# Optimization experiments

Hardware: AMD Instinct MI355X
Metric: run time of the kernel (lower is better)

The kernel has to match this reference:

```python
import jax, jax.numpy as jnp
import numpy as np

B, R, C, NC = 8, 1000, 1024, 81
H, W = 1024, 1024
MEANS = jnp.array([0.0, 0.0, 0.0, 0.0], jnp.float32)
STDS = jnp.array([0.1, 0.1, 0.2, 0.2], jnp.float32)
MIN_CONF = 0.05
NMS_THR = 0.5
MAX_INST = 100
NEG = -1e9


def setup_inputs() -> dict:
    key = jax.random.key(0)
    k1, k2, k3, k4, k5 = jax.random.split(key, 5)
    x = jax.random.normal(k1, (B * R, C), jnp.float32)
    w_cls = jax.random.normal(k2, (C, NC), jnp.float32) * 0.01
    b_cls = jnp.zeros((NC,), jnp.float32)
    w_delta = jax.random.normal(k3, (C, 4), jnp.float32) * 0.01
    b_delta = jnp.zeros((4,), jnp.float32)
    # rois: (batch_ind, y1, x1, y2, x2), normalized coords with y1<y2, x1<x2
    yx1 = jax.random.uniform(k4, (B * R, 2), jnp.float32) * 0.7
    hw = jax.random.uniform(k5, (B * R, 2), jnp.float32) * 0.28 + 0.02
    bind = jnp.repeat(jnp.arange(B, dtype=jnp.float32), R)[:, None]
    rois = jnp.concatenate([bind, yx1, yx1 + hw], axis=1)
    return {"x": x, "w_cls": w_cls, "b_cls": b_cls, "w_delta": w_delta, "b_delta": b_delta, "rois": rois}


def delta2bbox(rois, deltas):
    # rois, deltas: [N, 4] in (y1, x1, y2, x2) / (dy, dx, dh, dw)
    d = deltas * STDS + MEANS
    h = rois[:, 2] - rois[:, 0]
    w = rois[:, 3] - rois[:, 1]
    cy = rois[:, 0] + 0.5 * h + d[:, 0] * h
    cx = rois[:, 1] + 0.5 * w + d[:, 1] * w
    h = h * jnp.exp(d[:, 2])
    w = w * jnp.exp(d[:, 3])
    return jnp.stack([cy - 0.5 * h, cx - 0.5 * w, cy + 0.5 * h, cx + 0.5 * w], axis=1)


def pairwise_iou(boxes):
    # boxes: [N, 4]
    area = (boxes[:, 2] - boxes[:, 0]) * (boxes[:, 3] - boxes[:, 1])
    y1 = jnp.maximum(boxes[:, None, 0], boxes[None, :, 0])
    x1 = jnp.maximum(boxes[:, None, 1], boxes[None, :, 1])
    y2 = jnp.minimum(boxes[:, None, 2], boxes[None, :, 2])
    x2 = jnp.minimum(boxes[:, None, 3], boxes[None, :, 3])
    inter = jnp.maximum(y2 - y1, 0.0) * jnp.maximum(x2 - x1, 0.0)
    union = area[:, None] + area[None, :] - inter
    return inter / jnp.maximum(union, 1e-8)


def nms_single(boxes, scores, class_ids, valid):
    # boxes [R,4], scores [R], class_ids [R] int, valid [R] bool -> detections [MAX_INST, 6]
    masked = jnp.where(valid, scores, NEG)
    order = jnp.argsort(-masked)  # descending score
    b = boxes[order]
    s = masked[order]
    c = class_ids[order]
    v = valid[order]
    # class-aware IoU: cross-class pairs never suppress each other
    iou = pairwise_iou(b) * (c[:, None] == c[None, :]).astype(boxes.dtype)
    n = b.shape[0]

    def step(supp, xs):
        i, iou_row, vi = xs
        keep_i = vi & ~supp[i]
        supp = supp | jnp.where(keep_i, iou_row > NMS_THR, False)
        return supp, keep_i

    _, keep = jax.lax.scan(step, jnp.zeros((n,), bool), (jnp.arange(n), iou, v))
    final = jnp.where(keep, s, NEG)
    top_s, top_i = jax.lax.top_k(final, MAX_INST)
    ok = (top_s > NEG / 2)[:, None]
    det = jnp.concatenate([b[top_i], c[top_i].astype(boxes.dtype)[:, None], s[top_i][:, None]], axis=1)
    return jnp.where(ok, det, 0.0)


def reference(x, w_cls, b_cls, w_delta, b_delta, rois):
    logits = x @ w_cls + b_cls                      # [B*R, NC]
    probs = jax.nn.softmax(logits, axis=-1)
    deltas = x @ w_delta + b_delta                  # [B*R, 4]

    probs_b = probs.reshape(B, R, NC)
    class_ids = jnp.argmax(probs_b, axis=-1).astype(jnp.int32)           # [B, R]
    class_scores = jnp.take_along_axis(probs_b, class_ids[..., None], axis=-1)[..., 0]

    scale = jnp.array([H, W, H, W], jnp.float32)
    boxes = rois[:, 1:5] * scale                    # pixel coords, [B*R, 4]
    refined = delta2bbox(boxes, deltas)
    window = jnp.array([0.0, 0.0, float(H), float(W)], jnp.float32)
    refined = jnp.clip(refined, window[jnp.array([0, 1, 0, 1])], window[jnp.array([2, 3, 2, 3])])
    refined = refined.reshape(B, R, 4)

    valid = (class_ids > 0) & (class_scores >= MIN_CONF)
    detections = jax.vmap(nms_single)(refined, class_scores, class_ids, valid)  # [B, MAX_INST, 6]
    return detections
```

## Files before the change

kernel.cpp:

```cpp
#include <hip/hip_runtime.h>
#include <math.h>
#include <stdint.h>

#define RR 1000
#define CC 1024
#define NCLS 81
#define HH 1024.0f
#define MIN_CONF_V 0.05f
#define NMS_THR_V 0.5f
#define NEGV -1e9f

#define KSTRIDE 520

typedef __attribute__((ext_vector_type(8))) short bf16x8;
typedef __attribute__((ext_vector_type(16))) float f32x16;

__device__ __forceinline__ unsigned short f2bf(float f) {
    unsigned int u = __float_as_uint(f);
    return (unsigned short)((u + 0x7FFFu + ((u >> 16) & 1u)) >> 16);
}
__device__ __forceinline__ float bf2f(unsigned short h) {
    return __uint_as_float(((unsigned int)h) << 16);
}

__global__ __launch_bounds__(64) void k0_pack(
    const float* __restrict__ w_cls, const float* __restrict__ w_delta,
    unsigned short* __restrict__ wh, unsigned short* __restrict__ wl)
{
    const int ct = blockIdx.x >> 6;
    const int ks = blockIdx.x & 63;
    const int l = threadIdx.x;
    const int col = ct * 32 + (l & 31);
    const int kbase = ks * 16 + (l >> 5) * 8;
    unsigned short h[8], lo[8];
    #pragma unroll
    for (int j = 0; j < 8; ++j) {
        const int k = kbase + j;
        float v = 0.f;
        if (col < NCLS)          v = w_cls[(size_t)k * NCLS + col];
        else if (col < NCLS + 4) v = w_delta[(size_t)k * 4 + (col - NCLS)];
        h[j] = f2bf(v);
        lo[j] = f2bf(v - bf2f(h[j]));
    }
    const size_t base = ((size_t)(ct * 64 + ks) * 64 + l) * 8;
    uint4 uh, ul;
    uh.x = (unsigned)h[0] | ((unsigned)h[1] << 16);
    uh.y = (unsigned)h[2] | ((unsigned)h[3] << 16);
    uh.z = (unsigned)h[4] | ((unsigned)h[5] << 16);
    uh.w = (unsigned)h[6] | ((unsigned)h[7] << 16);
    ul.x = (unsigned)lo[0] | ((unsigned)lo[1] << 16);
    ul.y = (unsigned)lo[2] | ((unsigned)lo[3] << 16);
    ul.z = (unsigned)lo[4] | ((unsigned)lo[5] << 16);
    ul.w = (unsigned)lo[6] | ((unsigned)lo[7] << 16);
    *(uint4*)&wh[base] = uh;
    *(uint4*)&wl[base] = ul;
}

__global__ __launch_bounds__(384) void k1_head(
    const float* __restrict__ x,
    const unsigned short* __restrict__ wh, const unsigned short* __restrict__ wl,
    const float* __restrict__ b_cls, const float* __restrict__ b_delta,
    const float* __restrict__ rois,
    float* __restrict__ bx_ws, float* __restrict__ sc_ws, float* __restrict__ cid_ws)
{
    __shared__ __align__(16) unsigned short XH[64 * KSTRIDE];
    __shared__ __align__(16) unsigned short XL[64 * KSTRIDE];

    const int t = threadIdx.x;
    const int lane = t & 63;
    const int wid = t >> 6;
    const int ct = wid >> 1;
    const int half = wid & 1;
    const int row0 = blockIdx.x * 32;

    #pragma unroll
    for (int batch = 0; batch < 2; ++batch) {
        float4 v[11];
        #pragma unroll
        for (int i = 0; i < 11; ++i) {
            const int s = t + (batch * 11 + i) * 384;
            if (s < 8192)
                v[i] = *(const float4*)(x + (size_t)(row0 + (s >> 8)) * CC + (s & 255) * 4);
        }
        #pragma unroll
        for (int i = 0; i < 11; ++i) {
            const int s = t + (batch * 11 + i) * 384;
            if (s < 8192) {
                const int row = s >> 8;
                const int f4 = s & 255;
                const int ks = f4 >> 2;
                const int q = f4 & 3;
                const int lane_ = ((q >> 1) << 5) + row;
                const int j0 = (q & 1) * 4;
                const size_t us = (size_t)ks * KSTRIDE + lane_ * 8 + j0;
                const unsigned short h0 = f2bf(v[i].x), h1 = f2bf(v[i].y),
                                     h2 = f2bf(v[i].z), h3 = f2bf(v[i].w);
                *(ushort4*)&XH[us] = make_ushort4(h0, h1, h2, h3);
                *(ushort4*)&XL[us] = make_ushort4(
                    f2bf(v[i].x - bf2f(h0)), f2bf(v[i].y - bf2f(h1)),
                    f2bf(v[i].z - bf2f(h2)), f2bf(v[i].w - bf2f(h3)));
            }
        }
    }
    __syncthreads();

    const int ks0 = half * 32;
    const unsigned short* whp = wh + (((size_t)ct * 64 + ks0) * 64 + lane) * 8;
    const unsigned short* wlp = wl + (((size_t)ct * 64 + ks0) * 64 + lane) * 8;
    const unsigned short* ap  = &XH[(size_t)ks0 * KSTRIDE + lane * 8];
    const unsigned short* alp = &XL[(size_t)ks0 * KSTRIDE + lane * 8];

    f32x16 acc = {0.f,0.f,0.f,0.f,0.f,0.f,0.f,0.f,0.f,0.f,0.f,0.f,0.f,0.f,0.f,0.f};

    bf16x8 BH[4], BL[4];
    #pragma unroll
    for (int i = 0; i < 4; ++i) {
        BH[i] = *(const bf16x8*)(whp + (size_t)i * 512);
        BL[i] = *(const bf16x8*)(wlp + (size_t)i * 512);
    }

    #pragma unroll
    for (int ks = 0; ks < 32; ++ks) {
        const bf16x8 bh = BH[ks & 3];
        const bf16x8 bl = BL[ks & 3];
        if (ks + 4 < 32) {
            BH[ks & 3] = *(const bf16x8*)(whp + (size_t)(ks + 4) * 512);
            BL[ks & 3] = *(const bf16x8*)(wlp + (size_t)(ks + 4) * 512);
        }
        const bf16x8 ah = *(const bf16x8*)(ap  + (size_t)ks * KSTRIDE);
        const bf16x8 al = *(const bf16x8*)(alp + (size_t)ks * KSTRIDE);
        acc = __builtin_amdgcn_mfma_f32_32x32x16_bf16(ah, bh, acc, 0, 0, 0);
        acc = __builtin_amdgcn_mfma_f32_32x32x16_bf16(ah, bl, acc, 0, 0, 0);
        acc = __builtin_amdgcn_mfma_f32_32x32x16_bf16(al, bh, acc, 0, 0, 0);
    }
    __syncthreads();

    float* outH = (float*)XH;
    float* outT = outH + 3200;
    float* dst = half ? outT : outH;
    const int col = lane & 31;
    #pragma unroll
    for (int reg = 0; reg < 16; ++reg) {
        const int row = (reg & 3) + 8 * (reg >> 2) + 4 * (lane >> 5);
        dst[row * 100 + ct * 32 + col] = acc[reg];
    }
    __syncthreads();

    if (t < 256) {
        const int row = t >> 3;
        const int e = t & 7;
        float vmax = -INFINITY;
        int imax = 1 << 20;
        float vv[12];
        #pragma unroll
        for (int s = 0; s < 12; ++s) {
            const int cidx = e + 8 * s;
            if (cidx < NCLS) {
                const float val = outH[row * 100 + cidx] + outT[row * 100 + cidx] + b_cls[cidx];
                vv[s] = val;
                if (val > vmax) { vmax = val; imax = cidx; }
            } else vv[s] = -INFINITY;
        }
        #pragma unroll
        for (int mm = 4; mm >= 1; mm >>= 1) {
            const float v2 = __shfl_xor(vmax, mm);
            const int   i2 = __shfl_xor(imax, mm);
            if (v2 > vmax || (v2 == vmax && i2 < imax)) { vmax = v2; imax = i2; }
        }
        float sume = 0.f;
        #pragma unroll
        for (int s = 0; s < 12; ++s) {
            const int cidx = e + 8 * s;
            if (cidx < NCLS) sume += expf(vv[s] - vmax);
        }
        #pragma unroll
        for (int mm = 4; mm >= 1; mm >>= 1) sume += __shfl_xor(sume, mm);

        if (e == 0) {
            const int gr = row0 + row;
            const float score = 1.0f / sume;
            const int cid = imax;
            const float d0 = (outH[row * 100 + 81] + outT[row * 100 + 81] + b_delta[0]) * 0.1f;
            const float d1 = (outH[row * 100 + 82] + outT[row * 100 + 82] + b_delta[1]) * 0.1f;
            const float d2 = (outH[row * 100 + 83] + outT[row * 100 + 83] + b_delta[2]) * 0.2f;
            const float d3 = (outH[row * 100 + 84] + outT[row * 100 + 84] + b_delta[3]) * 0.2f;
            const float y1 = rois[(size_t)gr * 5 + 1] * HH;
            const float x1 = rois[(size_t)gr * 5 + 2] * HH;
            const float y2 = rois[(size_t)gr * 5 + 3] * HH;
            const float x2 = rois[(size_t)gr * 5 + 4] * HH;
            const float h = y2 - y1, w = x2 - x1;
            const float cy = y1 + 0.5f * h + d0 * h;
            const float cx = x1 + 0.5f * w + d1 * w;
            const float h2 = h * expf(d2);
            const float w2 = w * expf(d3);
            const float by1 = fminf(fmaxf(cy - 0.5f * h2, 0.f), HH);
            const float bx1 = fminf(fmaxf(cx - 0.5f * w2, 0.f), HH);
            const float by2 = fminf(fmaxf(cy + 0.5f * h2, 0.f), HH);
            const float bx2 = fminf(fmaxf(cx + 0.5f * w2, 0.f), HH);
            const bool valid = (cid > 0) && (score >= MIN_CONF_V);
            bx_ws[(size_t)gr * 4 + 0] = by1;
            bx_ws[(size_t)gr * 4 + 1] = bx1;
            bx_ws[(size_t)gr * 4 + 2] = by2;
            bx_ws[(size_t)gr * 4 + 3] = bx2;
            sc_ws[gr]  = valid ? score : NEGV;
            cid_ws[gr] = (float)cid;
        }
    }
}

__global__ __launch_bounds__(256) void k2_nms(
    const float* __restrict__ bx_ws, const float* __restrict__ sc_ws,
    const float* __restrict__ cid_ws, float* __restrict__ det)
{
    __shared__ unsigned long long keys[256];
    __shared__ float sy1[256], sx1[256], sy2[256], sx2[256];
    __shared__ float scl[256], ssc[256];
    __shared__ unsigned char supp[256];
    __shared__ int s_cnt, s_num;

    const int b = blockIdx.x;
    const int t = threadIdx.x;
    const int base = b * RR;

    keys[t] = 0ull;
    if (t == 0) { s_cnt = 0; s_num = 0; }
    __syncthreads();

    for (int rr = t; rr < RR; rr += 256) {
        const float s = sc_ws[base + rr];
        if (s > NEGV * 0.5f) {
            const int i = atomicAdd(&s_num, 1);
            if (i < 256) {
                unsigned int u = __float_as_uint(s) | 0x80000000u;
                keys[i] = ((unsigned long long)u << 32) | (unsigned int)(~(unsigned int)rr);
            }
        }
    }
    __syncthreads();
    const int V = (s_num < 256) ? s_num : 256;

    for (int k = 2; k <= 256; k <<= 1) {
        for (int j = k >> 1; j > 0; j >>= 1) {
            const int ixj = t ^ j;
            if (ixj > t) {
                const unsigned long long a = keys[t];
                const unsigned long long c = keys[ixj];
                const bool desc = ((t & k) == 0);
                if (desc ? (a < c) : (a > c)) { keys[t] = c; keys[ixj] = a; }
            }
            __syncthreads();
        }
    }

    if (t < V) {
        const int orig = (int)(~(unsigned int)keys[t]);
        const int g = base + orig;
        sy1[t] = bx_ws[(size_t)g * 4 + 0];
        sx1[t] = bx_ws[(size_t)g * 4 + 1];
        sy2[t] = bx_ws[(size_t)g * 4 + 2];
        sx2[t] = bx_ws[(size_t)g * 4 + 3];
        scl[t] = cid_ws[g];
        ssc[t] = sc_ws[g];
    } else {
        sy1[t] = sx1[t] = sy2[t] = sx2[t] = 0.f;
        scl[t] = -1.f;
        ssc[t] = NEGV;
    }
    supp[t] = 0;
    __syncthreads();

    for (int i = 0; i < V; ++i) {
        __syncthreads();
        if (s_cnt >= 100) break;
        if (!supp[i]) {
            if (t > i && t < V && scl[t] == scl[i]) {
                const float yy1 = fmaxf(sy1[i], sy1[t]);
                const float xx1 = fmaxf(sx1[i], sx1[t]);
                const float yy2 = fminf(sy2[i], sy2[t]);
                const float xx2 = fminf(sx2[i], sx2[t]);
                const float inter = fmaxf(yy2 - yy1, 0.f) * fmaxf(xx2 - xx1, 0.f);
                const float ai = (sy2[i] - sy1[i]) * (sx2[i] - sx1[i]);
                const float at = (sy2[t] - sy1[t]) * (sx2[t] - sx1[t]);
                const float uni = ai + at - inter;
                if (inter / fmaxf(uni, 1e-8f) > NMS_THR_V) supp[t] = 1;
            }
            if (t == 0) {
                const int slot = s_cnt;
                if (slot < 100) {
                    float* o = det + ((size_t)b * 100 + slot) * 6;
                    o[0] = sy1[i]; o[1] = sx1[i]; o[2] = sy2[i]; o[3] = sx2[i];
                    o[4] = scl[i]; o[5] = ssc[i];
                }
                s_cnt = slot + 1;
            }
        }
    }
    __syncthreads();
    int cnt = s_cnt;
    if (cnt > 100) cnt = 100;
    for (int idx = t; idx < 600; idx += 256) {
        if (idx >= cnt * 6) det[(size_t)b * 600 + idx] = 0.f;
    }
}

extern "C" void kernel_launch(void* const* d_in, const int* in_sizes, int n_in,
                              void* d_out, int out_size, void* d_ws, size_t ws_size,
                              hipStream_t stream) {
    const float* x       = (const float*)d_in[0];
    const float* w_cls   = (const float*)d_in[1];
    const float* b_cls   = (const float*)d_in[2];
    const float* w_delta = (const float*)d_in[3];
    const float* b_delta = (const float*)d_in[4];
    const float* rois    = (const float*)d_in[5];
    float* out = (float*)d_out;

    float* bx_ws   = (float*)d_ws;
    float* sc_ws   = bx_ws + 8000 * 4;
    float* cid_ws  = sc_ws + 8000;
    unsigned short* wh = (unsigned short*)(cid_ws + 8000);
    unsigned short* wl = wh + 98304;

    k0_pack<<<192, 64, 0, stream>>>(w_cls, w_delta, wh, wl);
    k1_head<<<250, 384, 0, stream>>>(x, wh, wl, b_cls, b_delta, rois,
                                     bx_ws, sc_ws, cid_ws);
    k2_nms<<<8, 256, 0, stream>>>(bx_ws, sc_ws, cid_ws, out);
}
```

Before: 30.70 us.

## Fuse pack, head GEMM and NMS into one cooperative kernel with grid syncs

Merges the three separate launches (weight packing, MFMA head with softmax and box decode, per-image NMS) into a single cooperative kernel of 250 blocks, separated by grid-wide barriers. NMS runs on the first 8 blocks and reuses the head's shared memory buffer. The goal is to remove two kernel launch gaps and their inter-kernel drain. In exchange it adds two grid.sync costs and leaves 242 blocks idle during NMS, and it requires all 250 blocks to be co-resident.

After: 80.49 us. +162.2%, slower.

```diff
diff --git a/kernel.cpp b/kernel.cpp
--- a/kernel.cpp
+++ b/kernel.cpp
@@ -1,6 +1,9 @@
 #include <hip/hip_runtime.h>
+#include <hip/hip_cooperative_groups.h>
 #include <math.h>
 #include <stdint.h>
+
+namespace cg = cooperative_groups;
 
 #define RR 1000
 #define CC 1024
@@ -23,283 +26,300 @@
     return __uint_as_float(((unsigned int)h) << 16);
 }
 
-__global__ __launch_bounds__(64) void k0_pack(
+__global__ __launch_bounds__(384, 1) void fused_all(
+    const float* __restrict__ x,
     const float* __restrict__ w_cls, const float* __restrict__ w_delta,
-    unsigned short* __restrict__ wh, unsigned short* __restrict__ wl)
-{
-    const int ct = blockIdx.x >> 6;
-    const int ks = blockIdx.x & 63;
-    const int l = threadIdx.x;
-    const int col = ct * 32 + (l & 31);
-    const int kbase = ks * 16 + (l >> 5) * 8;
-    unsigned short h[8], lo[8];
-    #pragma unroll
-    for (int j = 0; j < 8; ++j) {
-        const int k = kbase + j;
-        float v = 0.f;
-        if (col < NCLS)          v = w_cls[(size_t)k * NCLS + col];
-        else if (col < NCLS + 4) v = w_delta[(size_t)k * 4 + (col - NCLS)];
-        h[j] = f2bf(v);
-        lo[j] = f2bf(v - bf2f(h[j]));
-    }
-    const size_t base = ((size_t)(ct * 64 + ks) * 64 + l) * 8;
-    uint4 uh, ul;
-    uh.x = (unsigned)h[0] | ((unsigned)h[1] << 16);
-    uh.y = (unsigned)h[2] | ((unsigned)h[3] << 16);
-    uh.z = (unsigned)h[4] | ((unsigned)h[5] << 16);
-    uh.w = (unsigned)h[6] | ((unsigned)h[7] << 16);
-    ul.x = (unsigned)lo[0] | ((unsigned)lo[1] << 16);
-    ul.y = (unsigned)lo[2] | ((unsigned)lo[3] << 16);
-    ul.z = (unsigned)lo[4] | ((unsigned)lo[5] << 16);
-    ul.w = (unsigned)lo[6] | ((unsigned)lo[7] << 16);
-    *(uint4*)&wh[base] = uh;
-    *(uint4*)&wl[base] = ul;
-}
-
-__global__ __launch_bounds__(384) void k1_head(
-    const float* __restrict__ x,
-    const unsigned short* __restrict__ wh, const unsigned short* __restrict__ wl,
     const float* __restrict__ b_cls, const float* __restrict__ b_delta,
     const float* __restrict__ rois,
-    float* __restrict__ bx_ws, float* __restrict__ sc_ws, float* __restrict__ cid_ws)
+    unsigned short* __restrict__ wh, unsigned short* __restrict__ wl,
+    float* __restrict__ bx_ws, float* __restrict__ sc_ws, float* __restrict__ cid_ws,
+    float* __restrict__ det)
 {
     __shared__ __align__(16) unsigned short XH[64 * KSTRIDE];
     __shared__ __align__(16) unsigned short XL[64 * KSTRIDE];
 
     const int t = threadIdx.x;
-    const int lane = t & 63;
-    const int wid = t >> 6;
-    const int ct = wid >> 1;
-    const int half = wid & 1;
-    const int row0 = blockIdx.x * 32;
-
-    #pragma unroll
-    for (int batch = 0; batch < 2; ++batch) {
-        float4 v[11];
+    const int b = blockIdx.x;
+    cg::grid_group grid = cg::this_grid();
+
+    {
+        const int g = b * 384 + t;
+        if (g < 12288) {
+            const int lane = g & 63;
+            const int blk = g >> 6;
+            const int ct = blk >> 6;
+            const int ks = blk & 63;
+            const int col = ct * 32 + (lane & 31);
+            const int kbase = ks * 16 + (lane >> 5) * 8;
+            unsigned short h[8], lo[8];
+            #pragma unroll
+            for (int j = 0; j < 8; ++j) {
+                const int k = kbase + j;
+                float v = 0.f;
+                if (col < NCLS)          v = w_cls[(size_t)k * NCLS + col];
+                else if (col < NCLS + 4) v = w_delta[(size_t)k * 4 + (col - NCLS)];
+                h[j] = f2bf(v);
+                lo[j] = f2bf(v - bf2f(h[j]));
+            }
+            const size_t base = ((size_t)blk * 64 + lane) * 8;
+            uint4 uh, ul;
+            uh.x = (unsigned)h[0] | ((unsigned)h[1] << 16);
+            uh.y = (unsigned)h[2] | ((unsigned)h[3] << 16);
+            uh.z = (unsigned)h[4] | ((unsigned)h[5] << 16);
+            uh.w = (unsigned)h[6] | ((unsigned)h[7] << 16);
+            ul.x = (unsigned)lo[0] | ((unsigned)lo[1] << 16);
+            ul.y = (unsigned)lo[2] | ((unsigned)lo[3] << 16);
+            ul.z = (unsigned)lo[4] | ((unsigned)lo[5] << 16);
+            ul.w = (unsigned)lo[6] | ((unsigned)lo[7] << 16);
+            *(uint4*)&wh[base] = uh;
+            *(uint4*)&wl[base] = ul;
+        }
+    }
+    grid.sync();
+
+    {
+        const int lane = t & 63;
+        const int wid = t >> 6;
+        const int ct = wid >> 1;
+        const int half = wid & 1;
+        const int row0 = b * 32;
+
         #pragma unroll
-        for (int i = 0; i < 11; ++i) {
-            const int s = t + (batch * 11 + i) * 384;
-            if (s < 8192)
-                v[i] = *(const float4*)(x + (size_t)(row0 + (s >> 8)) * CC + (s & 255) * 4);
-        }
+        for (int batch = 0; batch < 2; ++batch) {
+            float4 v[11];
+            #pragma unroll
+            for (int i = 0; i < 11; ++i) {
+                const int s = t + (batch * 11 + i) * 384;
+                if (s < 8192)
+                    v[i] = *(const float4*)(x + (size_t)(row0 + (s >> 8)) * CC + (s & 255) * 4);
+            }
+            #pragma unroll
+            for (int i = 0; i < 11; ++i) {
+                const int s = t + (batch * 11 + i) * 384;
+                if (s < 8192) {
+                    const int row = s >> 8;
+                    const int f4 = s & 255;
+                    const int ks = f4 >> 2;
+                    const int q = f4 & 3;
+                    const int lane_ = ((q >> 1) << 5) + row;
+                    const int j0 = (q & 1) * 4;
+                    const size_t us = (size_t)ks * KSTRIDE + lane_ * 8 + j0;
+                    const unsigned short h0 = f2bf(v[i].x), h1 = f2bf(v[i].y),
+                                         h2 = f2bf(v[i].z), h3 = f2bf(v[i].w);
+                    *(ushort4*)&XH[us] = make_ushort4(h0, h1, h2, h3);
+                    *(ushort4*)&XL[us] = make_ushort4(
+                        f2bf(v[i].x - bf2f(h0)), f2bf(v[i].y - bf2f(h1)),
+                        f2bf(v[i].z - bf2f(h2)), f2bf(v[i].w - bf2f(h3)));
+                }
+            }
+        }
+        __syncthreads();
+
+        const int ks0 = half * 32;
+        const unsigned short* whp = wh + (((size_t)ct * 64 + ks0) * 64 + lane) * 8;
+        const unsigned short* wlp = wl + (((size_t)ct * 64 + ks0) * 64 + lane) * 8;
+        const unsigned short* ap  = &XH[(size_t)ks0 * KSTRIDE + lane * 8];
+        const unsigned short* alp = &XL[(size_t)ks0 * KSTRIDE + lane * 8];
+
+        f32x16 acc = {0.f,0.f,0.f,0.f,0.f,0.f,0.f,0.f,0.f,0.f,0.f,0.f,0.f,0.f,0.f,0.f};
+
+        bf16x8 BH[4], BL[4];
         #pragma unroll
-        for (int i = 0; i < 11; ++i) {
-            const int s = t + (batch * 11 + i) * 384;
-            if (s < 8192) {
-                const int row = s >> 8;
-                const int f4 = s & 255;
-                const int ks = f4 >> 2;
-                const int q = f4 & 3;
-                const int lane_ = ((q >> 1) << 5) + row;
-                const int j0 = (q & 1) * 4;
-                const size_t us = (size_t)ks * KSTRIDE + lane_ * 8 + j0;
-                const unsigned short h0 = f2bf(v[i].x), h1 = f2bf(v[i].y),
-                                     h2 = f2bf(v[i].z), h3 = f2bf(v[i].w);
-                *(ushort4*)&XH[us] = make_ushort4(h0, h1, h2, h3);
-                *(ushort4*)&XL[us] = make_ushort4(
-                    f2bf(v[i].x - bf2f(h0)), f2bf(v[i].y - bf2f(h1)),
-                    f2bf(v[i].z - bf2f(h2)), f2bf(v[i].w - bf2f(h3)));
+        for (int i = 0; i < 4; ++i) {
+            BH[i] = *(const bf16x8*)(whp + (size_t)i * 512);
+            BL[i] = *(const bf16x8*)(wlp + (size_t)i * 512);
+        }
+
+        #pragma unroll
+        for (int ks = 0; ks < 32; ++ks) {
+            const bf16x8 bh = BH[ks & 3];
+            const bf16x8 bl = BL[ks & 3];
+            if (ks + 4 < 32) {
+                BH[ks & 3] = *(const bf16x8*)(whp + (size_t)(ks + 4) * 512);
+                BL[ks & 3] = *(const bf16x8*)(wlp + (size_t)(ks + 4) * 512);
+            }
+            const bf16x8 ah = *(const bf16x8*)(ap  + (size_t)ks * KSTRIDE);
+            const bf16x8 al = *(const bf16x8*)(alp + (size_t)ks * KSTRIDE);
+            acc = __builtin_amdgcn_mfma_f32_32x32x16_bf16(ah, bh, acc, 0, 0, 0);
+            acc = __builtin_amdgcn_mfma_f32_32x32x16_bf16(ah, bl, acc, 0, 0, 0);
+            acc = __builtin_amdgcn_mfma_f32_32x32x16_bf16(al, bh, acc, 0, 0, 0);
+        }
+        __syncthreads();
+
+        float* outH = (float*)XH;
+        float* outT = outH + 3200;
+        float* dst = half ? outT : outH;
+        const int col = lane & 31;
+        #pragma unroll
+        for (int reg = 0; reg < 16; ++reg) {
+            const int row = (reg & 3) + 8 * (reg >> 2) + 4 * (lane >> 5);
+            dst[row * 100 + ct * 32 + col] = acc[reg];
+        }
+        __syncthreads();
+
+        if (t < 256) {
+            const int row = t >> 3;
+            const int e = t & 7;
+            float vmax = -INFINITY;
+            int imax = 1 << 20;
+            float vv[12];
+            #pragma unroll
+            for (int s = 0; s < 12; ++s) {
+                const int cidx = e + 8 * s;
+                if (cidx < NCLS) {
+                    const float val = outH[row * 100 + cidx] + outT[row * 100 + cidx] + b_cls[cidx];
+                    vv[s] = val;
+                    if (val > vmax) { vmax = val; imax = cidx; }
+                } else vv[s] = -INFINITY;
+            }
+            #pragma unroll
+            for (int mm = 4; mm >= 1; mm >>= 1) {
+                const float v2 = __shfl_xor(vmax, mm);
+                const int   i2 = __shfl_xor(imax, mm);
+                if (v2 > vmax || (v2 == vmax && i2 < imax)) { vmax = v2; imax = i2; }
+            }
+            float sume = 0.f;
+            #pragma unroll
+            for (int s = 0; s < 12; ++s) {
+                const int cidx = e + 8 * s;
+                if (cidx < NCLS) sume += expf(vv[s] - vmax);
+            }
+            #pragma unroll
+            for (int mm = 4; mm >= 1; mm >>= 1) sume += __shfl_xor(sume, mm);
+
+            if (e == 0) {
+                const int gr = row0 + row;
+                const float score = 1.0f / sume;
+                const int cid = imax;
+                const float d0 = (outH[row * 100 + 81] + outT[row * 100 + 81] + b_delta[0]) * 0.1f;
+                const float d1 = (outH[row * 100 + 82] + outT[row * 100 + 82] + b_delta[1]) * 0.1f;
+                const float d2 = (outH[row * 100 + 83] + outT[row * 100 + 83] + b_delta[2]) * 0.2f;
+                const float d3 = (outH[row * 100 + 84] + outT[row * 100 + 84] + b_delta[3]) * 0.2f;
+                const float y1 = rois[(size_t)gr * 5 + 1] * HH;
+                const float x1 = rois[(size_t)gr * 5 + 2] * HH;
+                const float y2 = rois[(size_t)gr * 5 + 3] * HH;
+                const float x2 = rois[(size_t)gr * 5 + 4] * HH;
+                const float h = y2 - y1, w = x2 - x1;
+                const float cy = y1 + 0.5f * h + d0 * h;
+                const float cx = x1 + 0.5f * w + d1 * w;
+                const float h2 = h * expf(d2);
+                const float w2 = w * expf(d3);
+                const float by1 = fminf(fmaxf(cy - 0.5f * h2, 0.f), HH);
+                const float bx1 = fminf(fmaxf(cx - 0.5f * w2, 0.f), HH);
+                const float by2 = fminf(fmaxf(cy + 0.5f * h2, 0.f), HH);
+                const float bx2 = fminf(fmaxf(cx + 0.5f * w2, 0.f), HH);
+                const bool valid = (cid > 0) && (score >= MIN_CONF_V);
+                bx_ws[(size_t)gr * 4 + 0] = by1;
+                bx_ws[(size_t)gr * 4 + 1] = bx1;
+                bx_ws[(size_t)gr * 4 + 2] = by2;
+                bx_ws[(size_t)gr * 4 + 3] = bx2;
+                sc_ws[gr]  = valid ? score : NEGV;
+                cid_ws[gr] = (float)cid;
             }
         }
     }
-    __syncthreads();
-
-    const int ks0 = half * 32;
-    const unsigned short* whp = wh + (((size_t)ct * 64 + ks0) * 64 + lane) * 8;
-    const unsigned short* wlp = wl + (((size_t)ct * 64 + ks0) * 64 + lane) * 8;
-    const unsigned short* ap  = &XH[(size_t)ks0 * KSTRIDE + lane * 8];
-    const unsigned short* alp = &XL[(size_t)ks0 * KSTRIDE + lane * 8];
-
-    f32x16 acc = {0.f,0.f,0.f,0.f,0.f,0.f,0.f,0.f,0.f,0.f,0.f,0.f,0.f,0.f,0.f,0.f};
-
-    bf16x8 BH[4], BL[4];
-    #pragma unroll
-    for (int i = 0; i < 4; ++i) {
-        BH[i] = *(const bf16x8*)(whp + (size_t)i * 512);
-        BL[i] = *(const bf16x8*)(wlp + (size_t)i * 512);
-    }
-
-    #pragma unroll
-    for (int ks = 0; ks < 32; ++ks) {
-        const bf16x8 bh = BH[ks & 3];
-        const bf16x8 bl = BL[ks & 3];
-        if (ks + 4 < 32) {
-            BH[ks & 3] = *(const bf16x8*)(whp + (size_t)(ks + 4) * 512);
-            BL[ks & 3] = *(const bf16x8*)(wlp + (size_t)(ks + 4) * 512);
-        }
-        const bf16x8 ah = *(const bf16x8*)(ap  + (size_t)ks * KSTRIDE);
-        const bf16x8 al = *(const bf16x8*)(alp + (size_t)ks * KSTRIDE);
-        acc = __builtin_amdgcn_mfma_f32_32x32x16_bf16(ah, bh, acc, 0, 0, 0);
-        acc = __builtin_amdgcn_mfma_f32_32x32x16_bf16(ah, bl, acc, 0, 0, 0);
-        acc = __builtin_amdgcn_mfma_f32_32x32x16_bf16(al, bh, acc, 0, 0, 0);
-    }
-    __syncthreads();
-
-    float* outH = (float*)XH;
-    float* outT = outH + 3200;
-    float* dst = half ? outT : outH;
-    const int col = lane & 31;
-    #pragma unroll
-    for (int reg = 0; reg < 16; ++reg) {
-        const int row = (reg & 3) + 8 * (reg >> 2) + 4 * (lane >> 5);
-        dst[row * 100 + ct * 32 + col] = acc[reg];
-    }
-    __syncthreads();
-
-    if (t < 256) {
-        const int row = t >> 3;
-        const int e = t & 7;
-        float vmax = -INFINITY;
-        int imax = 1 << 20;
-        float vv[12];
-        #pragma unroll
-        for (int s = 0; s < 12; ++s) {
-            const int cidx = e + 8 * s;
-            if (cidx < NCLS) {
-                const float val = outH[row * 100 + cidx] + outT[row * 100 + cidx] + b_cls[cidx];
-                vv[s] = val;
-                if (val > vmax) { vmax = val; imax = cidx; }
-            } else vv[s] = -INFINITY;
-        }
-        #pragma unroll
-        for (int mm = 4; mm >= 1; mm >>= 1) {
-            const float v2 = __shfl_xor(vmax, mm);
-            const int   i2 = __shfl_xor(imax, mm);
-            if (v2 > vmax || (v2 == vmax && i2 < imax)) { vmax = v2; imax = i2; }
-        }
-        float sume = 0.f;
-        #pragma unroll
-        for (int s = 0; s < 12; ++s) {
-            const int cidx = e + 8 * s;
-            if (cidx < NCLS) sume += expf(vv[s] - vmax);
-        }
-        #pragma unroll
-        for (int mm = 4; mm >= 1; mm >>= 1) sume += __shfl_xor(sume, mm);
-
-        if (e == 0) {
-            const int gr = row0 + row;
-            const float score = 1.0f / sume;
-            const int cid = imax;
-            const float d0 = (outH[row * 100 + 81] + outT[row * 100 + 81] + b_delta[0]) * 0.1f;
-            const float d1 = (outH[row * 100 + 82] + outT[row * 100 + 82] + b_delta[1]) * 0.1f;
-            const float d2 = (outH[row * 100 + 83] + outT[row * 100 + 83] + b_delta[2]) * 0.2f;
-            const float d3 = (outH[row * 100 + 84] + outT[row * 100 + 84] + b_delta[3]) * 0.2f;
-            const float y1 = rois[(size_t)gr * 5 + 1] * HH;
-            const float x1 = rois[(size_t)gr * 5 + 2] * HH;
-            const float y2 = rois[(size_t)gr * 5 + 3] * HH;
-            const float x2 = rois[(size_t)gr * 5 + 4] * HH;
-            const float h = y2 - y1, w = x2 - x1;
-            const float cy = y1 + 0.5f * h + d0 * h;
-            const float cx = x1 + 0.5f * w + d1 * w;
-            const float h2 = h * expf(d2);
-            const float w2 = w * expf(d3);
-            const float by1 = fminf(fmaxf(cy - 0.5f * h2, 0.f), HH);
-            const float bx1 = fminf(fmaxf(cx - 0.5f * w2, 0.f), HH);
-            const float by2 = fminf(fmaxf(cy + 0.5f * h2, 0.f), HH);
-            const float bx2 = fminf(fmaxf(cx + 0.5f * w2, 0.f), HH);
-            const bool valid = (cid > 0) && (score >= MIN_CONF_V);
-            bx_ws[(size_t)gr * 4 + 0] = by1;
-            bx_ws[(size_t)gr * 4 + 1] = bx1;
-            bx_ws[(size_t)gr * 4 + 2] = by2;
-            bx_ws[(size_t)gr * 4 + 3] = bx2;
-            sc_ws[gr]  = valid ? score : NEGV;
-            cid_ws[gr] = (float)cid;
-        }
-    }
-}
-
-__global__ __launch_bounds__(256) void k2_nms(
-    const float* __restrict__ bx_ws, const float* __restrict__ sc_ws,
-    const float* __restrict__ cid_ws, float* __restrict__ det)
-{
-    __shared__ unsigned long long keys[256];
-    __shared__ float sy1[256], sx1[256], sy2[256], sx2[256];
-    __shared__ float scl[256], ssc[256];
-    __shared__ unsigned char supp[256];
-    __shared__ int s_cnt, s_num;
-
-    const int b = blockIdx.x;
-    const int t = threadIdx.x;
-    const int base = b * RR;
-
-    keys[t] = 0ull;
-    if (t == 0) { s_cnt = 0; s_num = 0; }
-    __syncthreads();
-
-    for (int rr = t; rr < RR; rr += 256) {
-        const float s = sc_ws[base + rr];
-        if (s > NEGV * 0.5f) {
-            const int i = atomicAdd(&s_num, 1);
-            if (i < 256) {
-                unsigned int u = __float_as_uint(s) | 0x80000000u;
-                keys[i] = ((unsigned long long)u << 32) | (unsigned int)(~(unsigned int)rr);
-            }
-        }
-    }
-    __syncthreads();
-    const int V = (s_num < 256) ? s_num : 256;
-
-    for (int k = 2; k <= 256; k <<= 1) {
-        for (int j = k >> 1; j > 0; j >>= 1) {
-            const int ixj = t ^ j;
-            if (ixj > t) {
-                const unsigned long long a = keys[t];
-                const unsigned long long c = keys[ixj];
-                const bool desc = ((t & k) == 0);
-                if (desc ? (a < c) : (a > c)) { keys[t] = c; keys[ixj] = a; }
-            }
+    grid.sync();
+
+    if (b < 8) {
+        float* fb = (float*)XH;
+        unsigned long long* keys = (unsigned long long*)fb;
+        float* sy1 = fb + 512;
+        float* sx1 = fb + 768;
+        float* sy2 = fb + 1024;
+        float* sx2 = fb + 1280;
+        float* scl = fb + 1536;
+        float* ssc = fb + 1792;
+        unsigned char* supp = (unsigned char*)(fb + 2048);
+        int* s_cnt = (int*)(fb + 2112);
+        int* s_num = (int*)(fb + 2113);
+
+        const int base = b * RR;
+
+        if (t < 256) keys[t] = 0ull;
+        if (t == 0) { *s_cnt = 0; *s_num = 0; }
+        __syncthreads();
+
+        for (int rr = t; rr < RR; rr += 384) {
+            const float s = sc_ws[base + rr];
+            if (s > NEGV * 0.5f) {
+                const int i = atomicAdd(s_num, 1);
+                if (i < 256) {
+                    unsigned int u = __float_as_uint(s) | 0x80000000u;
+                    keys[i] = ((unsigned long long)u << 32) | (unsigned int)(~(unsigned int)rr);
+                }
+            }
+        }
+        __syncthreads();
+        const int V = (*s_num < 256) ? *s_num : 256;
+
+        if (V > 1) {
+            for (int k = 2; k <= 256; k <<= 1) {
+                for (int j = k >> 1; j > 0; j >>= 1) {
+                    if (t < 256) {
+                        const int ixj = t ^ j;
+                        if (ixj > t) {
+                            const unsigned long long a = keys[t];
+                            const unsigned long long c = keys[ixj];
+                            const bool desc = ((t & k) == 0);
+                            if (desc ? (a < c) : (a > c)) { keys[t] = c; keys[ixj] = a; }
+                        }
+                    }
+                    __syncthreads();
+                }
+            }
+        }
+
+        if (t < 256) {
+            if (t < V) {
+                const int orig = (int)(~(unsigned int)keys[t]);
+                const int g = base + orig;
+                sy1[t] = bx_ws[(size_t)g * 4 + 0];
+                sx1[t] = bx_ws[(size_t)g * 4 + 1];
+                sy2[t] = bx_ws[(size_t)g * 4 + 2];
+                sx2[t] = bx_ws[(size_t)g * 4 + 3];
+                scl[t] = cid_ws[g];
+                ssc[t] = sc_ws[g];
+            } else {
+                sy1[t] = sx1[t] = sy2[t] = sx2[t] = 0.f;
+                scl[t] = -1.f;
+                ssc[t] = NEGV;
+            }
+            supp[t] = 0;
+        }
+        __syncthreads();
+
+        for (int i = 0; i < V; ++i) {
             __syncthreads();
-        }
-    }
-
-    if (t < V) {
-        const int orig = (int)(~(unsigned int)keys[t]);
-        const int g = base + orig;
-        sy1[t] = bx_ws[(size_t)g * 4 + 0];
-        sx1[t] = bx_ws[(size_t)g * 4 + 1];
-        sy2[t] = bx_ws[(size_t)g * 4 + 2];
-        sx2[t] = bx_ws[(size_t)g * 4 + 3];
-        scl[t] = cid_ws[g];
-        ssc[t] = sc_ws[g];
-    } else {
-        sy1[t] = sx1[t] = sy2[t] = sx2[t] = 0.f;
-        scl[t] = -1.f;
-        ssc[t] = NEGV;
-    }
-    supp[t] = 0;
-    __syncthreads();
-
-    for (int i = 0; i < V; ++i) {
-        __syncthreads();
-        if (s_cnt >= 100) break;
-        if (!supp[i]) {
-            if (t > i && t < V && scl[t] == scl[i]) {
-                const float yy1 = fmaxf(sy1[i], sy1[t]);
-                const float xx1 = fmaxf(sx1[i], sx1[t]);
-                const float yy2 = fminf(sy2[i], sy2[t]);
-                const float xx2 = fminf(sx2[i], sx2[t]);
-                const float inter = fmaxf(yy2 - yy1, 0.f) * fmaxf(xx2 - xx1, 0.f);
-                const float ai = (sy2[i] - sy1[i]) * (sx2[i] - sx1[i]);
-                const float at = (sy2[t] - sy1[t]) * (sx2[t] - sx1[t]);
-                const float uni = ai + at - inter;
-                if (inter / fmaxf(uni, 1e-8f) > NMS_THR_V) supp[t] = 1;
-            }
-            if (t == 0) {
-                const int slot = s_cnt;
-                if (slot < 100) {
-                    float* o = det + ((size_t)b * 100 + slot) * 6;
-                    o[0] = sy1[i]; o[1] = sx1[i]; o[2] = sy2[i]; o[3] = sx2[i];
-                    o[4] = scl[i]; o[5] = ssc[i];
-                }
-                s_cnt = slot + 1;
-            }
-        }
-    }
-    __syncthreads();
-    int cnt = s_cnt;
-    if (cnt > 100) cnt = 100;
-    for (int idx = t; idx < 600; idx += 256) {
-        if (idx >= cnt * 6) det[(size_t)b * 600 + idx] = 0.f;
+            if (*s_cnt >= 100) break;
+            if (!supp[i]) {
+                if (t > i && t < V && scl[t] == scl[i]) {
+                    const float yy1 = fmaxf(sy1[i], sy1[t]);
+                    const float xx1 = fmaxf(sx1[i], sx1[t]);
+                    const float yy2 = fminf(sy2[i], sy2[t]);
+                    const float xx2 = fminf(sx2[i], sx2[t]);
+                    const float inter = fmaxf(yy2 - yy1, 0.f) * fmaxf(xx2 - xx1, 0.f);
+                    const float ai = (sy2[i] - sy1[i]) * (sx2[i] - sx1[i]);
+                    const float at = (sy2[t] - sy1[t]) * (sx2[t] - sx1[t]);
+                    const float uni = ai + at - inter;
+                    if (inter / fmaxf(uni, 1e-8f) > NMS_THR_V) supp[t] = 1;
+                }
+                if (t == 0) {
+                    const int slot = *s_cnt;
+                    if (slot < 100) {
+                        float* o = det + ((size_t)b * 100 + slot) * 6;
+                        o[0] = sy1[i]; o[1] = sx1[i]; o[2] = sy2[i]; o[3] = sx2[i];
+                        o[4] = scl[i]; o[5] = ssc[i];
+                    }
+                    *s_cnt = slot + 1;
+                }
+            }
+        }
+        __syncthreads();
+        int cnt = *s_cnt;
+        if (cnt > 100) cnt = 100;
+        for (int idx = t; idx < 600; idx += 384) {
+            if (idx >= cnt * 6) det[(size_t)b * 600 + idx] = 0.f;
+        }
     }
 }
 
@@ -312,7 +332,7 @@
     const float* w_delta = (const float*)d_in[3];
     const float* b_delta = (const float*)d_in[4];
     const float* rois    = (const float*)d_in[5];
-    float* out = (float*)d_out;
+    float* det = (float*)d_out;
 
     float* bx_ws   = (float*)d_ws;
     float* sc_ws   = bx_ws + 8000 * 4;
@@ -320,8 +340,11 @@
     unsigned short* wh = (unsigned short*)(cid_ws + 8000);
     unsigned short* wl = wh + 98304;
 
-    k0_pack<<<192, 64, 0, stream>>>(w_cls, w_delta, wh, wl);
-    k1_head<<<250, 384, 0, stream>>>(x, wh, wl, b_cls, b_delta, rois,
-                                     bx_ws, sc_ws, cid_ws);
-    k2_nms<<<8, 256, 0, stream>>>(bx_ws, sc_ws, cid_ws, out);
+    void* args[] = {
+        (void*)&x, (void*)&w_cls, (void*)&w_delta, (void*)&b_cls, (void*)&b_delta,
+        (void*)&rois, (void*)&wh, (void*)&wl,
+        (void*)&bx_ws, (void*)&sc_ws, (void*)&cid_ws, (void*)&det
+    };
+    hipLaunchCooperativeKernel((const void*)fused_all, dim3(250), dim3(384),
+                               args, 0, stream);
 }
```
